# Kernel optimization log

Hardware: AMD Instinct MI355X
Metric: run time of the kernel (lower is better)

## Reference

```python
import jax, jax.numpy as jnp
import numpy as np

LAYERS = 30
LAYERS_PER_STACK = 10  # layers // stacks
UPSAMPLE_SCALES = (10, 8)


def _c1x1(w, x):
    # 1x1 conv: w [O,C], x [B,C,T] -> [B,O,T]
    return jnp.einsum('oc,bct->bot', w, x)


def setup_inputs() -> dict:
    key = jax.random.key(0)
    ks = jax.random.split(key, 16)
    B, T, F = 4, 32000, 400
    s = 0.1  # weight scale to keep gates unsaturated
    inp = {
        'x': jax.random.normal(ks[0], (B, 256, T), jnp.float32),
        'c': jax.random.normal(ks[1], (B, 80, F), jnp.float32),
        'first_w': jax.random.normal(ks[2], (64, 256), jnp.float32) * s,
        'first_b': jnp.zeros((64,), jnp.float32),
        'conv_w': jax.random.normal(ks[3], (LAYERS, 128, 64, 2), jnp.float32) * s,
        'conv_b': jnp.zeros((LAYERS, 128), jnp.float32),
        'cond_w': jax.random.normal(ks[4], (LAYERS, 128, 80), jnp.float32) * s,
        'out_w': jax.random.normal(ks[5], (LAYERS, 64, 64), jnp.float32) * s,
        'out_b': jnp.zeros((LAYERS, 64), jnp.float32),
        'skip_w': jax.random.normal(ks[6], (LAYERS, 64, 64), jnp.float32) * s,
        'skip_b': jnp.zeros((LAYERS, 64), jnp.float32),
        'last1_w': jax.random.normal(ks[7], (64, 64), jnp.float32) * s,
        'last1_b': jnp.zeros((64,), jnp.float32),
        'last2_w': jax.random.normal(ks[8], (256, 64), jnp.float32) * s,
        'last2_b': jnp.zeros((256,), jnp.float32),
        'conv_in_w': jax.random.normal(ks[9], (80, 80), jnp.float32) * s,
        # upsample smoothing kernels, torch init: constant 1/kernel_size
        'up_w0': jnp.full((2 * 10 + 1,), 1.0 / (2 * 10 + 1), jnp.float32),
        'up_w1': jnp.full((2 * 8 + 1,), 1.0 / (2 * 8 + 1), jnp.float32),
    }
    return inp


def _wavenet(x, c, first_w, first_b, conv_w, conv_b, cond_w, out_w, out_b,
             skip_w, skip_b, last1_w, last1_b, last2_w, last2_b, conv_in_w,
             up_w0, up_w1):
    # --- ConvInUpsampleNetwork (aux_context_window=0 -> conv_in is 1x1, no bias) ---
    c = _c1x1(conv_in_w, c)  # [B,80,F]
    C = c.shape[1]
    for scale, w in zip(UPSAMPLE_SCALES, (up_w0, up_w1)):
        c = jnp.repeat(c, scale, axis=2)  # nearest interpolate along time
        rhs = jnp.broadcast_to(w[None, None, :], (C, 1, w.shape[0]))  # depthwise avg
        c = jax.lax.conv_general_dilated(
            c, rhs, window_strides=(1,), padding=[(scale, scale)],
            feature_group_count=C, dimension_numbers=('NCH', 'OIH', 'NCH'))
    # c now [B,80,T] with T = F*80 matching x
    T = x.shape[2]

    # --- first 1x1 conv ---
    h = _c1x1(first_w, x) + first_b[None, :, None]  # [B,64,T]

    skips = jnp.zeros_like(h[:, :64, :]) * 0.0  # [B,64,T]
    skips = 0.0
    for l in range(LAYERS):
        d = 2 ** (l % LAYERS_PER_STACK)  # dilation; padding = (k-1)*d = d
        xp = jnp.pad(h, ((0, 0), (0, 0), (d, 0)))  # causal left pad
        # dilated conv, kernel_size=2: taps at t-d and t
        g = (jnp.einsum('oc,bct->bot', conv_w[l, :, :, 0], xp[:, :, :T])
             + jnp.einsum('oc,bct->bot', conv_w[l, :, :, 1], xp[:, :, d:d + T])
             + conv_b[l][None, :, None])  # [B,128,T]
        g = g + _c1x1(cond_w[l], c)  # conditioning (split(a,b)+split(ca,cb) == split(g+cc))
        a, b = jnp.split(g, 2, axis=1)
        z = jnp.tanh(a) * jax.nn.sigmoid(b)  # [B,64,T]
        skips = skips + _c1x1(skip_w[l], z) + skip_b[l][None, :, None]
        h = h + _c1x1(out_w[l], z) + out_b[l][None, :, None]

    # --- last conv layers: ReLU, 1x1, ReLU, 1x1 ---
    o = jax.nn.relu(skips)
    o = _c1x1(last1_w, o) + last1_b[None, :, None]
    o = jax.nn.relu(o)
    o = _c1x1(last2_w, o) + last2_b[None, :, None]
    return o  # [B,256,T]


def reference(x, c, first_w, first_b, conv_w, conv_b, cond_w, out_w, out_b,
              skip_w, skip_b, last1_w, last1_b, last2_w, last2_b, conv_in_w,
              up_w0, up_w1):
    return _wavenet(x, c, first_w, first_b, conv_w, conv_b, cond_w, out_w,
                    out_b, skip_w, skip_b, last1_w, last1_b, last2_w, last2_b,
                    conv_in_w, up_w0, up_w1)
```

## Files before the change

### kernel.cpp

```cpp
#include <hip/hip_runtime.h>
#include <math.h>

#define T_TOTAL 32000
#define BATCH 4
#define TT 64

typedef __bf16 bf16x8 __attribute__((ext_vector_type(8)));
typedef float f32x4 __attribute__((ext_vector_type(4)));
typedef unsigned int uint4v __attribute__((ext_vector_type(4)));
typedef unsigned int uint2v __attribute__((ext_vector_type(2)));

__device__ __forceinline__ unsigned short f2b(float f) {
    unsigned int u = __float_as_uint(f);
    u += 0x7FFFu + ((u >> 16) & 1u);
    return (unsigned short)(u >> 16);
}
__device__ __forceinline__ unsigned int f2b2(float lo, float hi) {
    return (unsigned int)f2b(lo) | ((unsigned int)f2b(hi) << 16);
}
__device__ __forceinline__ bf16x8 ld_bf8(const unsigned short* p) {
    return __builtin_bit_cast(bf16x8, *(const uint4v*)p);
}
__device__ __forceinline__ float fast_sigmoid(float x) {
    return __builtin_amdgcn_rcpf(1.0f + __expf(-x));
}
__device__ __forceinline__ float fast_tanh(float x) {
    return 1.0f - 2.0f * __builtin_amdgcn_rcpf(1.0f + __expf(2.0f * x));
}

__global__ void k_pack(const float* __restrict__ conv_w, const float* __restrict__ cond_w,
                       const float* __restrict__ skip_w, const float* __restrict__ out_w,
                       const float* __restrict__ first_w, const float* __restrict__ last1_w,
                       const float* __restrict__ last2_w,
                       unsigned short* __restrict__ wgp, unsigned short* __restrict__ wzp,
                       unsigned short* __restrict__ fwp, unsigned short* __restrict__ l1p,
                       unsigned short* __restrict__ l2p) {
    int i = blockIdx.x * blockDim.x + threadIdx.x;
    if (i < 860160) {
        int l = i / 28672, r = i % 28672;
        int o = r / 224, k = r % 224;
        float v;
        if (k < 64)       v = conv_w[(((size_t)l * 128 + o) * 64 + k) * 2 + 0];
        else if (k < 128) v = conv_w[(((size_t)l * 128 + o) * 64 + (k - 64)) * 2 + 1];
        else if (k < 208) v = cond_w[((size_t)l * 128 + o) * 80 + (k - 128)];
        else              v = 0.0f;
        wgp[i] = f2b(v);
        return;
    }
    i -= 860160;
    if (i < 245760) {
        int l = i / 8192, rr = (i % 8192) / 64, k = i % 64;
        float v = (rr < 64) ? skip_w[((size_t)l * 64 + rr) * 64 + k]
                            : out_w[((size_t)l * 64 + (rr - 64)) * 64 + k];
        wzp[i] = f2b(v);
        return;
    }
    i -= 245760;
    if (i < 16384) { fwp[i] = f2b(first_w[i]); return; }
    i -= 16384;
    if (i < 4096) { l1p[i] = f2b(last1_w[i]); return; }
    i -= 4096;
    if (i < 16384) { l2p[i] = f2b(last2_w[i]); return; }
}

__global__ void k_convin(const float* __restrict__ c, const float* __restrict__ w,
                         float* __restrict__ c1) {
    int idx = blockIdx.x * blockDim.x + threadIdx.x;
    if (idx >= BATCH * 80 * 400) return;
    int f = idx % 400;
    int o = (idx / 400) % 80;
    int b = idx / (400 * 80);
    const float* cb = c + (size_t)b * 80 * 400 + f;
    const float* wr = w + o * 80;
    float acc = 0.f;
    #pragma unroll 8
    for (int j = 0; j < 80; ++j) acc += wr[j] * cb[(size_t)j * 400];
    c1[idx] = acc;
}

__global__ void k_up0(const float* __restrict__ c1, const float* __restrict__ w,
                      float* __restrict__ c2) {
    int idx = blockIdx.x * blockDim.x + threadIdx.x;
    if (idx >= BATCH * 80 * 4000) return;
    int t = idx % 4000;
    int ch = idx / 4000;
    int u = t / 10, r = t - u * 10;
    float w0 = 0.f, w1 = 0.f, w2 = 0.f;
    #pragma unroll
    for (int j = 0; j < 21; ++j) {
        float wj = w[j];
        int a = r - 10 + j;
        if (a < 0) w0 += wj;
        else if (a < 10) w1 += wj;
        else w2 += wj;
    }
    const float* src = c1 + (size_t)ch * 400;
    float s0 = (u >= 1) ? src[u - 1] : 0.f;
    float s1 = src[u];
    float s2 = (u + 1 < 400) ? src[u + 1] : 0.f;
    c2[idx] = w0 * s0 + w1 * s1 + w2 * s2;
}

__global__ __launch_bounds__(256) void k_up1b(const float* __restrict__ c2,
                                              const float* __restrict__ w,
                                              unsigned short* __restrict__ cupb) {
    __shared__ float S[80][13];
    __shared__ float W[8][4];
    const int b = blockIdx.y, t0 = blockIdx.x * 64;
    const int tid = threadIdx.x;
    const int u0 = t0 >> 3;

    for (int i = tid; i < 800; i += 256) {
        int ch = i / 10, uu = i % 10;
        int u = u0 - 1 + uu;
        float v = 0.f;
        if (u >= 0 && u < 4000) v = c2[((size_t)b * 80 + ch) * 4000 + u];
        S[ch][uu] = v;
    }
    if (tid < 24) {
        int r = tid / 3, k = tid % 3;
        int jlo = (k == 0) ? 0 : (k == 1 ? 8 - r : 16 - r);
        int jhi = (k == 0) ? 7 - r : (k == 1 ? 15 - r : 16);
        float a = 0.f;
        for (int j = jlo; j <= jhi; ++j) a += w[j];
        W[r][k] = a;
    }
    __syncthreads();

    unsigned short* ob = cupb + ((size_t)b * T_TOTAL + t0) * 96;
    for (int i = tid; i < 64 * 96; i += 256) {
        int ch = i % 96;
        int tl = i / 96;
        float acc = 0.f;
        if (ch < 80) {
            int r = tl & 7, ub = tl >> 3;
            acc = W[r][0] * S[ch][ub] + W[r][1] * S[ch][ub + 1] + W[r][2] * S[ch][ub + 2];
        }
        ob[i] = f2b(acc);
    }
}

__global__ __launch_bounds__(256, 4) void k_first(
    const float* __restrict__ x, const unsigned short* __restrict__ fwp,
    const float* __restrict__ fb, float* __restrict__ h0) {
    __shared__ unsigned short Xf[64 * 264];
    const int b = blockIdx.y, t0 = blockIdx.x * TT, tid = threadIdx.x;
    const int lane = tid & 63;
    const int wv = __builtin_amdgcn_readfirstlane(tid >> 6);
    const int l15 = lane & 15, q = lane >> 4;

    for (int i = tid; i < 2048; i += 256) {
        int tb = i >> 8, ch = i & 255;
        const float* xr = x + ((size_t)b * 256 + ch) * T_TOTAL + t0 + tb * 8;
        float4 u0 = *(const float4*)xr;
        float4 u1 = *(const float4*)(xr + 4);
        int base = (tb * 8) * 264 + ch;
        Xf[base + 0 * 264] = f2b(u0.x);
        Xf[base + 1 * 264] = f2b(u0.y);
        Xf[base + 2 * 264] = f2b(u0.z);
        Xf[base + 3 * 264] = f2b(u0.w);
        Xf[base + 4 * 264] = f2b(u1.x);
        Xf[base + 5 * 264] = f2b(u1.y);
        Xf[base + 6 * 264] = f2b(u1.z);
        Xf[base + 7 * 264] = f2b(u1.w);
    }
    __syncthreads();

    f32x4 acc[4] = {};
    const unsigned short* wr = fwp + (size_t)(16 * wv + l15) * 256;
    #pragma unroll
    for (int ks = 0; ks < 8; ++ks) {
        bf16x8 aA = ld_bf8(wr + ks * 32 + q * 8);
        #pragma unroll
        for (int tt = 0; tt < 4; ++tt) {
            bf16x8 bb = ld_bf8(&Xf[(tt * 16 + l15) * 264 + ks * 32 + q * 8]);
            acc[tt] = __builtin_amdgcn_mfma_f32_16x16x32_bf16(aA, bb, acc[tt], 0, 0, 0);
        }
    }
    const float4 fbv = *(const float4*)&fb[16 * wv + 4 * q];
    float* hob = h0 + (size_t)b * T_TOTAL * 64;
    #pragma unroll
    for (int tt = 0; tt < 4; ++tt) {
        size_t base = (size_t)(t0 + tt * 16 + l15) * 64 + 16 * wv + 4 * q;
        float4 ho;
        ho.x = acc[tt][0] + fbv.x;
        ho.y = acc[tt][1] + fbv.y;
        ho.z = acc[tt][2] + fbv.z;
        ho.w = acc[tt][3] + fbv.w;
        *(float4*)(hob + base) = ho;
    }
}

__global__ __launch_bounds__(256, 4) void k_layer(
    const float* __restrict__ h_in, float* __restrict__ h_out,
    float* __restrict__ skips, const unsigned short* __restrict__ cupb,
    const unsigned short* __restrict__ wgp, const unsigned short* __restrict__ wzp,
    const float* __restrict__ cb_l, const float* __restrict__ ob_l,
    const float* __restrict__ sb_l, int d, int first) {
    __shared__ unsigned short Xl[64 * 224];
    __shared__ unsigned short zs[64 * 72];
    const int b = blockIdx.y, t0 = blockIdx.x * TT, tid = threadIdx.x;
    const int lane = tid & 63;
    const int wv = __builtin_amdgcn_readfirstlane(tid >> 6);
    const int l15 = lane & 15, q = lane >> 4;

    const float* hb = h_in + (size_t)b * T_TOTAL * 64;
    for (int i = tid; i < 512; i += 256) {
        int t = i >> 3, cb8 = (i & 7) << 3;
        const float4* p1 = (const float4*)(hb + (size_t)(t0 + t) * 64 + cb8);
        float4 u0 = p1[0], u1 = p1[1];
        uint4v v1;
        v1.x = f2b2(u0.x, u0.y); v1.y = f2b2(u0.z, u0.w);
        v1.z = f2b2(u1.x, u1.y); v1.w = f2b2(u1.z, u1.w);
        *(uint4v*)&Xl[t * 224 + 64 + cb8] = v1;
        int td = t0 + t - d;
        uint4v v0 = {0u, 0u, 0u, 0u};
        if (td >= 0) {
            const float4* p0 = (const float4*)(hb + (size_t)td * 64 + cb8);
            float4 w0 = p0[0], w1 = p0[1];
            v0.x = f2b2(w0.x, w0.y); v0.y = f2b2(w0.z, w0.w);
            v0.z = f2b2(w1.x, w1.y); v0.w = f2b2(w1.z, w1.w);
        }
        *(uint4v*)&Xl[t * 224 + cb8] = v0;
    }
    const unsigned short* cbb = cupb + (size_t)b * T_TOTAL * 96;
    for (int i = tid; i < 768; i += 256) {
        int t = i / 12, j = (i % 12) << 3;
        *(uint4v*)&Xl[t * 224 + 128 + j] = *(const uint4v*)&cbb[(size_t)(t0 + t) * 96 + j];
    }
    __syncthreads();

    f32x4 accA[4] = {}, accG[4] = {};
    const unsigned short* wrow_a = wgp + (size_t)(16 * wv + l15) * 224;
    const unsigned short* wrow_g = wgp + (size_t)(64 + 16 * wv + l15) * 224;
    #pragma unroll
    for (int ks = 0; ks < 7; ++ks) {
        bf16x8 aA = ld_bf8(wrow_a + ks * 32 + q * 8);
        bf16x8 aG = ld_bf8(wrow_g + ks * 32 + q * 8);
        #pragma unroll
        for (int tt = 0; tt < 4; ++tt) {
            bf16x8 bb = ld_bf8(&Xl[(tt * 16 + l15) * 224 + ks * 32 + q * 8]);
            accA[tt] = __builtin_amdgcn_mfma_f32_16x16x32_bf16(aA, bb, accA[tt], 0, 0, 0);
            accG[tt] = __builtin_amdgcn_mfma_f32_16x16x32_bf16(aG, bb, accG[tt], 0, 0, 0);
        }
    }
    const float4 cbA = *(const float4*)&cb_l[16 * wv + 4 * q];
    const float4 cbG = *(const float4*)&cb_l[64 + 16 * wv + 4 * q];
    #pragma unroll
    for (int tt = 0; tt < 4; ++tt) {
        int t = tt * 16 + l15;
        float z0 = fast_tanh(accA[tt][0] + cbA.x) * fast_sigmoid(accG[tt][0] + cbG.x);
        float z1 = fast_tanh(accA[tt][1] + cbA.y) * fast_sigmoid(accG[tt][1] + cbG.y);
        float z2 = fast_tanh(accA[tt][2] + cbA.z) * fast_sigmoid(accG[tt][2] + cbG.z);
        float z3 = fast_tanh(accA[tt][3] + cbA.w) * fast_sigmoid(accG[tt][3] + cbG.w);
        uint2v zv;
        zv.x = f2b2(z0, z1);
        zv.y = f2b2(z2, z3);
        *(uint2v*)&zs[t * 72 + 16 * wv + 4 * q] = zv;
    }
    __syncthreads();

    f32x4 accS[4] = {}, accO[4] = {};
    const unsigned short* zrow_s = wzp + (size_t)(16 * wv + l15) * 64;
    const unsigned short* zrow_o = wzp + (size_t)(64 + 16 * wv + l15) * 64;
    #pragma unroll
    for (int ks = 0; ks < 2; ++ks) {
        bf16x8 aS = ld_bf8(zrow_s + ks * 32 + q * 8);
        bf16x8 aO = ld_bf8(zrow_o + ks * 32 + q * 8);
        #pragma unroll
        for (int tt = 0; tt < 4; ++tt) {
            bf16x8 bb = ld_bf8(&zs[(tt * 16 + l15) * 72 + ks * 32 + q * 8]);
            accS[tt] = __builtin_amdgcn_mfma_f32_16x16x32_bf16(aS, bb, accS[tt], 0, 0, 0);
            accO[tt] = __builtin_amdgcn_mfma_f32_16x16x32_bf16(aO, bb, accO[tt], 0, 0, 0);
        }
    }
    const float4 sbv = *(const float4*)&sb_l[16 * wv + 4 * q];
    const float4 obv = *(const float4*)&ob_l[16 * wv + 4 * q];
    float* hob = h_out + (size_t)b * T_TOTAL * 64;
    float* skb = skips + (size_t)b * T_TOTAL * 64;
    #pragma unroll
    for (int tt = 0; tt < 4; ++tt) {
        size_t base = (size_t)(t0 + tt * 16 + l15) * 64 + 16 * wv + 4 * q;
        float4 hi = *(const float4*)(hb + base);
        float4 ho;
        ho.x = hi.x + accO[tt][0] + obv.x;
        ho.y = hi.y + accO[tt][1] + obv.y;
        ho.z = hi.z + accO[tt][2] + obv.z;
        ho.w = hi.w + accO[tt][3] + obv.w;
        *(float4*)(hob + base) = ho;
        float4 sv;
        if (first) {
            sv.x = accS[tt][0] + sbv.x;
            sv.y = accS[tt][1] + sbv.y;
            sv.z = accS[tt][2] + sbv.z;
            sv.w = accS[tt][3] + sbv.w;
        } else {
            float4 sp = *(const float4*)(skb + base);
            sv.x = sp.x + accS[tt][0] + sbv.x;
            sv.y = sp.y + accS[tt][1] + sbv.y;
            sv.z = sp.z + accS[tt][2] + sbv.z;
            sv.w = sp.w + accS[tt][3] + sbv.w;
        }
        *(float4*)(skb + base) = sv;
    }
}

__global__ __launch_bounds__(256) void k_last(
    const float* __restrict__ skips, const unsigned short* __restrict__ l1p,
    const float* __restrict__ b1, const unsigned short* __restrict__ l2p,
    const float* __restrict__ b2, float* __restrict__ out) {
    __shared__ unsigned short sp[64 * 72];
    __shared__ unsigned short o2s[64 * 72];
    const int b = blockIdx.y, t0 = blockIdx.x * TT, tid = threadIdx.x;
    const int lane = tid & 63;
    const int wv = __builtin_amdgcn_readfirstlane(tid >> 6);
    const int l15 = lane & 15, q = lane >> 4;

    const float* skb = skips + (size_t)b * T_TOTAL * 64;
    for (int i = tid; i < 512; i += 256) {
        int t = i >> 3, cb8 = (i & 7) << 3;
        const float4* p = (const float4*)(skb + (size_t)(t0 + t) * 64 + cb8);
        float4 u0 = p[0], u1 = p[1];
        uint4v v;
        v.x = f2b2(fmaxf(u0.x, 0.f), fmaxf(u0.y, 0.f));
        v.y = f2b2(fmaxf(u0.z, 0.f), fmaxf(u0.w, 0.f));
        v.z = f2b2(fmaxf(u1.x, 0.f), fmaxf(u1.y, 0.f));
        v.w = f2b2(fmaxf(u1.z, 0.f), fmaxf(u1.w, 0.f));
        *(uint4v*)&sp[t * 72 + cb8] = v;
    }
    __syncthreads();

    f32x4 a1[4] = {};
    const unsigned short* w1r = l1p + (size_t)(16 * wv + l15) * 64;
    #pragma unroll
    for (int ks = 0; ks < 2; ++ks) {
        bf16x8 aA = ld_bf8(w1r + ks * 32 + q * 8);
        #pragma unroll
        for (int tt = 0; tt < 4; ++tt) {
            bf16x8 bb = ld_bf8(&sp[(tt * 16 + l15) * 72 + ks * 32 + q * 8]);
            a1[tt] = __builtin_amdgcn_mfma_f32_16x16x32_bf16(aA, bb, a1[tt], 0, 0, 0);
        }
    }
    const float4 b1v = *(const float4*)&b1[16 * wv + 4 * q];
    #pragma unroll
    for (int tt = 0; tt < 4; ++tt) {
        int t = tt * 16 + l15;
        float z0 = fmaxf(a1[tt][0] + b1v.x, 0.f);
        float z1 = fmaxf(a1[tt][1] + b1v.y, 0.f);
        float z2 = fmaxf(a1[tt][2] + b1v.z, 0.f);
        float z3 = fmaxf(a1[tt][3] + b1v.w, 0.f);
        uint2v zv;
        zv.x = f2b2(z0, z1);
        zv.y = f2b2(z2, z3);
        *(uint2v*)&o2s[t * 72 + 16 * wv + 4 * q] = zv;
    }
    __syncthreads();

    f32x4 a2[4][4] = {};
    #pragma unroll
    for (int ks = 0; ks < 2; ++ks) {
        bf16x8 aw[4];
        #pragma unroll
        for (int j = 0; j < 4; ++j)
            aw[j] = ld_bf8(l2p + (size_t)(64 * wv + 16 * j + l15) * 64 + ks * 32 + q * 8);
        #pragma unroll
        for (int tt = 0; tt < 4; ++tt) {
            bf16x8 bb = ld_bf8(&o2s[(tt * 16 + l15) * 72 + ks * 32 + q * 8]);
            #pragma unroll
            for (int j = 0; j < 4; ++j)
                a2[j][tt] = __builtin_amdgcn_mfma_f32_16x16x32_bf16(aw[j], bb, a2[j][tt], 0, 0, 0);
        }
    }
    float* ob = out + (size_t)b * 256 * T_TOTAL;
    #pragma unroll
    for (int j = 0; j < 4; ++j) {
        int o0 = 64 * wv + 16 * j + 4 * q;
        float4 b2v = *(const float4*)&b2[o0];
        #pragma unroll
        for (int tt = 0; tt < 4; ++tt) {
            int t = t0 + tt * 16 + l15;
            ob[(size_t)(o0 + 0) * T_TOTAL + t] = a2[j][tt][0] + b2v.x;
            ob[(size_t)(o0 + 1) * T_TOTAL + t] = a2[j][tt][1] + b2v.y;
            ob[(size_t)(o0 + 2) * T_TOTAL + t] = a2[j][tt][2] + b2v.z;
            ob[(size_t)(o0 + 3) * T_TOTAL + t] = a2[j][tt][3] + b2v.w;
        }
    }
}

extern "C" void kernel_launch(void* const* d_in, const int* in_sizes, int n_in,
                              void* d_out, int out_size, void* d_ws, size_t ws_size,
                              hipStream_t stream) {
    const float* x         = (const float*)d_in[0];
    const float* c         = (const float*)d_in[1];
    const float* first_w   = (const float*)d_in[2];
    const float* first_b   = (const float*)d_in[3];
    const float* conv_w    = (const float*)d_in[4];
    const float* conv_b    = (const float*)d_in[5];
    const float* cond_w    = (const float*)d_in[6];
    const float* out_w     = (const float*)d_in[7];
    const float* out_b     = (const float*)d_in[8];
    const float* skip_w    = (const float*)d_in[9];
    const float* skip_b    = (const float*)d_in[10];
    const float* last1_w   = (const float*)d_in[11];
    const float* last1_b   = (const float*)d_in[12];
    const float* last2_w   = (const float*)d_in[13];
    const float* last2_b   = (const float*)d_in[14];
    const float* conv_in_w = (const float*)d_in[15];
    const float* up_w0     = (const float*)d_in[16];
    const float* up_w1     = (const float*)d_in[17];

    unsigned char* base = (unsigned char*)d_ws;
    float* c1            = (float*)(base + 0);
    float* c2            = (float*)(base + 512000);
    unsigned short* cupb = (unsigned short*)(base + 5632000);
    float* hA            = (float*)(base + 30208000);
    float* hB            = (float*)(base + 62976000);
    float* skips         = (float*)(base + 95744000);
    unsigned short* wgp  = (unsigned short*)(base + 128512000);
    unsigned short* wzp  = (unsigned short*)(base + 130232320);
    unsigned short* fwp  = (unsigned short*)(base + 130723840);
    unsigned short* l1p  = (unsigned short*)(base + 130756608);
    unsigned short* l2p  = (unsigned short*)(base + 130764800);

    k_pack<<<(1142784 + 255) / 256, 256, 0, stream>>>(
        conv_w, cond_w, skip_w, out_w, first_w, last1_w, last2_w,
        wgp, wzp, fwp, l1p, l2p);
    k_convin<<<(BATCH * 80 * 400 + 255) / 256, 256, 0, stream>>>(c, conv_in_w, c1);
    k_up0<<<(BATCH * 80 * 4000 + 255) / 256, 256, 0, stream>>>(c1, up_w0, c2);
    dim3 upg(T_TOTAL / 64, BATCH);
    k_up1b<<<upg, 256, 0, stream>>>(c2, up_w1, cupb);

    dim3 grid(T_TOTAL / TT, BATCH);
    k_first<<<grid, 256, 0, stream>>>(x, fwp, first_b, hA);

    float* hin = hA;
    float* hout = hB;
    for (int l = 0; l < 30; ++l) {
        int d = 1 << (l % 10);
        k_layer<<<grid, 256, 0, stream>>>(
            hin, hout, skips, cupb,
            wgp + (size_t)l * 128 * 224, wzp + (size_t)l * 128 * 64,
            conv_b + (size_t)l * 128, out_b + (size_t)l * 64, skip_b + (size_t)l * 64,
            d, l == 0 ? 1 : 0);
        float* tmp = hin; hin = hout; hout = tmp;
    }

    k_last<<<grid, 256, 0, stream>>>(skips, l1p, last1_b, l2p, last2_b, (float*)d_out);
}
```

Baseline: 1.504 ms.

## Defer skip projections to a final kernel using per-layer bf16 gate outputs

When the workspace is large enough, each layer kernel writes its gated activation z to a per-layer bf16 buffer instead of reading and writing the fp32 skips accumulator. A new k_skips kernel then accumulates all 30 skip projections in registers, adds the pre-summed skip bias, and runs the two output convolutions. This removes the per-layer fp32 read-modify-write of skips, at the cost of about 490 MB of extra workspace and one large final read. Separately, k_first loads one float4 per thread and pads its shared-memory row stride to 266 to reduce bank conflicts. If the workspace is too small, the old path is kept as a fallback.

Measured after the change: 1.493 ms. About the same (-0.7%).

```diff
diff --git a/kernel.cpp b/kernel.cpp
--- a/kernel.cpp
+++ b/kernel.cpp
@@ -31,10 +31,10 @@
 __global__ void k_pack(const float* __restrict__ conv_w, const float* __restrict__ cond_w,
                        const float* __restrict__ skip_w, const float* __restrict__ out_w,
                        const float* __restrict__ first_w, const float* __restrict__ last1_w,
-                       const float* __restrict__ last2_w,
+                       const float* __restrict__ last2_w, const float* __restrict__ skip_b,
                        unsigned short* __restrict__ wgp, unsigned short* __restrict__ wzp,
                        unsigned short* __restrict__ fwp, unsigned short* __restrict__ l1p,
-                       unsigned short* __restrict__ l2p) {
+                       unsigned short* __restrict__ l2p, float* __restrict__ sbs, int do_sbs) {
     int i = blockIdx.x * blockDim.x + threadIdx.x;
     if (i < 860160) {
         int l = i / 28672, r = i % 28672;
@@ -61,6 +61,12 @@
     if (i < 4096) { l1p[i] = f2b(last1_w[i]); return; }
     i -= 4096;
     if (i < 16384) { l2p[i] = f2b(last2_w[i]); return; }
+    i -= 16384;
+    if (i < 64 && do_sbs) {
+        float a = 0.f;
+        for (int l = 0; l < 30; ++l) a += skip_b[l * 64 + i];
+        sbs[i] = a;
+    }
 }
 
 __global__ void k_convin(const float* __restrict__ c, const float* __restrict__ w,
@@ -140,29 +146,26 @@
     }
 }
 
+#define XFS 266
 __global__ __launch_bounds__(256, 4) void k_first(
     const float* __restrict__ x, const unsigned short* __restrict__ fwp,
     const float* __restrict__ fb, float* __restrict__ h0) {
-    __shared__ unsigned short Xf[64 * 264];
+    __shared__ unsigned short Xf[64 * XFS];
     const int b = blockIdx.y, t0 = blockIdx.x * TT, tid = threadIdx.x;
     const int lane = tid & 63;
     const int wv = __builtin_amdgcn_readfirstlane(tid >> 6);
     const int l15 = lane & 15, q = lane >> 4;
 
-    for (int i = tid; i < 2048; i += 256) {
-        int tb = i >> 8, ch = i & 255;
-        const float* xr = x + ((size_t)b * 256 + ch) * T_TOTAL + t0 + tb * 8;
-        float4 u0 = *(const float4*)xr;
-        float4 u1 = *(const float4*)(xr + 4);
-        int base = (tb * 8) * 264 + ch;
-        Xf[base + 0 * 264] = f2b(u0.x);
-        Xf[base + 1 * 264] = f2b(u0.y);
-        Xf[base + 2 * 264] = f2b(u0.z);
-        Xf[base + 3 * 264] = f2b(u0.w);
-        Xf[base + 4 * 264] = f2b(u1.x);
-        Xf[base + 5 * 264] = f2b(u1.y);
-        Xf[base + 6 * 264] = f2b(u1.z);
-        Xf[base + 7 * 264] = f2b(u1.w);
+    for (int i = tid; i < 4096; i += 256) {
+        int ch = i >> 4;
+        int t4 = (i & 15) << 2;
+        const float* xr = x + ((size_t)b * 256 + ch) * T_TOTAL + t0 + t4;
+        float4 u = *(const float4*)xr;
+        int base = t4 * XFS + ch;
+        Xf[base + 0 * XFS] = f2b(u.x);
+        Xf[base + 1 * XFS] = f2b(u.y);
+        Xf[base + 2 * XFS] = f2b(u.z);
+        Xf[base + 3 * XFS] = f2b(u.w);
     }
     __syncthreads();
 
@@ -173,7 +176,7 @@
         bf16x8 aA = ld_bf8(wr + ks * 32 + q * 8);
         #pragma unroll
         for (int tt = 0; tt < 4; ++tt) {
-            bf16x8 bb = ld_bf8(&Xf[(tt * 16 + l15) * 264 + ks * 32 + q * 8]);
+            bf16x8 bb = ld_bf8(&Xf[(tt * 16 + l15) * XFS + ks * 32 + q * 8]);
             acc[tt] = __builtin_amdgcn_mfma_f32_16x16x32_bf16(aA, bb, acc[tt], 0, 0, 0);
         }
     }
@@ -192,6 +195,108 @@
 }
 
 __global__ __launch_bounds__(256, 4) void k_layer(
+    const float* __restrict__ h_in, float* __restrict__ h_out,
+    unsigned short* __restrict__ zb_l, const unsigned short* __restrict__ cupb,
+    const unsigned short* __restrict__ wgp_l, const unsigned short* __restrict__ wzp_l,
+    const float* __restrict__ cb_l, const float* __restrict__ ob_l, int d) {
+    __shared__ unsigned short Xl[64 * 224];
+    __shared__ unsigned short zs[64 * 72];
+    const int b = blockIdx.y, t0 = blockIdx.x * TT, tid = threadIdx.x;
+    const int lane = tid & 63;
+    const int wv = __builtin_amdgcn_readfirstlane(tid >> 6);
+    const int l15 = lane & 15, q = lane >> 4;
+
+    const float* hb = h_in + (size_t)b * T_TOTAL * 64;
+    for (int i = tid; i < 512; i += 256) {
+        int t = i >> 3, cb8 = (i & 7) << 3;
+        const float4* p1 = (const float4*)(hb + (size_t)(t0 + t) * 64 + cb8);
+        float4 u0 = p1[0], u1 = p1[1];
+        uint4v v1;
+        v1.x = f2b2(u0.x, u0.y); v1.y = f2b2(u0.z, u0.w);
+        v1.z = f2b2(u1.x, u1.y); v1.w = f2b2(u1.z, u1.w);
+        *(uint4v*)&Xl[t * 224 + 64 + cb8] = v1;
+        int td = t0 + t - d;
+        uint4v v0 = {0u, 0u, 0u, 0u};
+        if (td >= 0) {
+            const float4* p0 = (const float4*)(hb + (size_t)td * 64 + cb8);
+            float4 w0 = p0[0], w1 = p0[1];
+            v0.x = f2b2(w0.x, w0.y); v0.y = f2b2(w0.z, w0.w);
+            v0.z = f2b2(w1.x, w1.y); v0.w = f2b2(w1.z, w1.w);
+        }
+        *(uint4v*)&Xl[t * 224 + cb8] = v0;
+    }
+    const unsigned short* cbb = cupb + (size_t)b * T_TOTAL * 96;
+    for (int i = tid; i < 768; i += 256) {
+        int t = i / 12, j = (i % 12) << 3;
+        *(uint4v*)&Xl[t * 224 + 128 + j] = *(const uint4v*)&cbb[(size_t)(t0 + t) * 96 + j];
+    }
+    __syncthreads();
+
+    f32x4 accA[4] = {}, accG[4] = {};
+    const unsigned short* wrow_a = wgp_l + (size_t)(16 * wv + l15) * 224;
+    const unsigned short* wrow_g = wgp_l + (size_t)(64 + 16 * wv + l15) * 224;
+    #pragma unroll
+    for (int ks = 0; ks < 7; ++ks) {
+        bf16x8 aA = ld_bf8(wrow_a + ks * 32 + q * 8);
+        bf16x8 aG = ld_bf8(wrow_g + ks * 32 + q * 8);
+        #pragma unroll
+        for (int tt = 0; tt < 4; ++tt) {
+            bf16x8 bb = ld_bf8(&Xl[(tt * 16 + l15) * 224 + ks * 32 + q * 8]);
+            accA[tt] = __builtin_amdgcn_mfma_f32_16x16x32_bf16(aA, bb, accA[tt], 0, 0, 0);
+            accG[tt] = __builtin_amdgcn_mfma_f32_16x16x32_bf16(aG, bb, accG[tt], 0, 0, 0);
+        }
+    }
+    const float4 cbA = *(const float4*)&cb_l[16 * wv + 4 * q];
+    const float4 cbG = *(const float4*)&cb_l[64 + 16 * wv + 4 * q];
+    #pragma unroll
+    for (int tt = 0; tt < 4; ++tt) {
+        int t = tt * 16 + l15;
+        float z0 = fast_tanh(accA[tt][0] + cbA.x) * fast_sigmoid(accG[tt][0] + cbG.x);
+        float z1 = fast_tanh(accA[tt][1] + cbA.y) * fast_sigmoid(accG[tt][1] + cbG.y);
+        float z2 = fast_tanh(accA[tt][2] + cbA.z) * fast_sigmoid(accG[tt][2] + cbG.z);
+        float z3 = fast_tanh(accA[tt][3] + cbA.w) * fast_sigmoid(accG[tt][3] + cbG.w);
+        uint2v zv;
+        zv.x = f2b2(z0, z1);
+        zv.y = f2b2(z2, z3);
+        *(uint2v*)&zs[t * 72 + 16 * wv + 4 * q] = zv;
+    }
+    __syncthreads();
+
+    unsigned short* zg = zb_l + ((size_t)b * T_TOTAL + t0) * 64;
+    #pragma unroll
+    for (int it = 0; it < 2; ++it) {
+        int i = tid + it * 256;
+        int t = i >> 3, c8 = (i & 7) << 3;
+        *(uint4v*)&zg[t * 64 + c8] = *(const uint4v*)&zs[t * 72 + c8];
+    }
+
+    f32x4 accO[4] = {};
+    const unsigned short* zrow_o = wzp_l + (size_t)(64 + 16 * wv + l15) * 64;
+    #pragma unroll
+    for (int ks = 0; ks < 2; ++ks) {
+        bf16x8 aO = ld_bf8(zrow_o + ks * 32 + q * 8);
+        #pragma unroll
+        for (int tt = 0; tt < 4; ++tt) {
+            bf16x8 bb = ld_bf8(&zs[(tt * 16 + l15) * 72 + ks * 32 + q * 8]);
+            accO[tt] = __builtin_amdgcn_mfma_f32_16x16x32_bf16(aO, bb, accO[tt], 0, 0, 0);
+        }
+    }
+    const float4 obv = *(const float4*)&ob_l[16 * wv + 4 * q];
+    float* hob = h_out + (size_t)b * T_TOTAL * 64;
+    #pragma unroll
+    for (int tt = 0; tt < 4; ++tt) {
+        size_t base = (size_t)(t0 + tt * 16 + l15) * 64 + 16 * wv + 4 * q;
+        float4 hi = *(const float4*)(hb + base);
+        float4 ho;
+        ho.x = hi.x + accO[tt][0] + obv.x;
+        ho.y = hi.y + accO[tt][1] + obv.y;
+        ho.z = hi.z + accO[tt][2] + obv.z;
+        ho.w = hi.w + accO[tt][3] + obv.w;
+        *(float4*)(hob + base) = ho;
+    }
+}
+
+__global__ __launch_bounds__(256, 4) void k_layer_f(
     const float* __restrict__ h_in, float* __restrict__ h_out,
     float* __restrict__ skips, const unsigned short* __restrict__ cupb,
     const unsigned short* __restrict__ wgp, const unsigned short* __restrict__ wzp,
@@ -305,6 +410,113 @@
     }
 }
 
+__global__ __launch_bounds__(256) void k_skips(
+    const unsigned short* __restrict__ zbuf, const unsigned short* __restrict__ wzp,
+    const float* __restrict__ sbs, const unsigned short* __restrict__ l1p,
+    const float* __restrict__ b1, const unsigned short* __restrict__ l2p,
+    const float* __restrict__ b2, float* __restrict__ out) {
+    __shared__ unsigned short zt[64 * 72];
+    __shared__ unsigned short o2s[64 * 72];
+    const int b = blockIdx.y, t0 = blockIdx.x * TT, tid = threadIdx.x;
+    const int lane = tid & 63;
+    const int wv = __builtin_amdgcn_readfirstlane(tid >> 6);
+    const int l15 = lane & 15, q = lane >> 4;
+
+    const int st_t = tid >> 3, st_c = (tid & 7) << 3;
+    const int st_t2 = (tid + 256) >> 3, st_c2 = ((tid + 256) & 7) << 3;
+    const unsigned short* zb = zbuf + ((size_t)b * T_TOTAL + t0) * 64;
+
+    f32x4 acc[4] = {};
+    for (int l = 0; l < 30; ++l) {
+        const unsigned short* src = zb + (size_t)l * BATCH * T_TOTAL * 64;
+        *(uint4v*)&zt[st_t * 72 + st_c] = *(const uint4v*)&src[st_t * 64 + st_c];
+        *(uint4v*)&zt[st_t2 * 72 + st_c2] = *(const uint4v*)&src[st_t2 * 64 + st_c2];
+        __syncthreads();
+        const unsigned short* wr = wzp + (size_t)l * 8192 + (size_t)(16 * wv + l15) * 64;
+        #pragma unroll
+        for (int ks = 0; ks < 2; ++ks) {
+            bf16x8 aS = ld_bf8(wr + ks * 32 + q * 8);
+            #pragma unroll
+            for (int tt = 0; tt < 4; ++tt) {
+                bf16x8 bb = ld_bf8(&zt[(tt * 16 + l15) * 72 + ks * 32 + q * 8]);
+                acc[tt] = __builtin_amdgcn_mfma_f32_16x16x32_bf16(aS, bb, acc[tt], 0, 0, 0);
+            }
+        }
+        __syncthreads();
+    }
+
+    const float4 sbv = *(const float4*)&sbs[16 * wv + 4 * q];
+    #pragma unroll
+    for (int tt = 0; tt < 4; ++tt) {
+        int t = tt * 16 + l15;
+        float s0 = fmaxf(acc[tt][0] + sbv.x, 0.f);
+        float s1 = fmaxf(acc[tt][1] + sbv.y, 0.f);
+        float s2 = fmaxf(acc[tt][2] + sbv.z, 0.f);
+        float s3 = fmaxf(acc[tt][3] + sbv.w, 0.f);
+        uint2v zv;
+        zv.x = f2b2(s0, s1);
+        zv.y = f2b2(s2, s3);
+        *(uint2v*)&zt[t * 72 + 16 * wv + 4 * q] = zv;
+    }
+    __syncthreads();
+
+    f32x4 a1[4] = {};
+    const unsigned short* w1r = l1p + (size_t)(16 * wv + l15) * 64;
+    #pragma unroll
+    for (int ks = 0; ks < 2; ++ks) {
+        bf16x8 aA = ld_bf8(w1r + ks * 32 + q * 8);
+        #pragma unroll
+        for (int tt = 0; tt < 4; ++tt) {
+            bf16x8 bb = ld_bf8(&zt[(tt * 16 + l15) * 72 + ks * 32 + q * 8]);
+            a1[tt] = __builtin_amdgcn_mfma_f32_16x16x32_bf16(aA, bb, a1[tt], 0, 0, 0);
+        }
+    }
+    const float4 b1v = *(const float4*)&b1[16 * wv + 4 * q];
+    #pragma unroll
+    for (int tt = 0; tt < 4; ++tt) {
+        int t = tt * 16 + l15;
+        float z0 = fmaxf(a1[tt][0] + b1v.x, 0.f);
+        float z1 = fmaxf(a1[tt][1] + b1v.y, 0.f);
+        float z2 = fmaxf(a1[tt][2] + b1v.z, 0.f);
+        float z3 = fmaxf(a1[tt][3] + b1v.w, 0.f);
+        uint2v zv;
+        zv.x = f2b2(z0, z1);
+        zv.y = f2b2(z2, z3);
+        *(uint2v*)&o2s[t * 72 + 16 * wv + 4 * q] = zv;
+    }
+    __syncthreads();
+
+    f32x4 a2[4][4] = {};
+    #pragma unroll
+    for (int ks = 0; ks < 2; ++ks) {
+        bf16x8 aw[4];
+        #pragma unroll
+        for (int j = 0; j < 4; ++j)
+            aw[j] = ld_bf8(l2p + (size_t)(64 * wv + 16 * j + l15) * 64 + ks * 32 + q * 8);
+        #pragma unroll
+        for (int tt = 0; tt < 4; ++tt) {
+            bf16x8 bb = ld_bf8(&o2s[(tt * 16 + l15) * 72 + ks * 32 + q * 8]);
+            #pragma unroll
+            for (int j = 0; j < 4; ++j)
+                a2[j][tt] = __builtin_amdgcn_mfma_f32_16x16x32_bf16(aw[j], bb, a2[j][tt], 0, 0, 0);
+        }
+    }
+    float* ob = out + (size_t)b * 256 * T_TOTAL;
+    #pragma unroll
+    for (int j = 0; j < 4; ++j) {
+        int o0 = 64 * wv + 16 * j + 4 * q;
+        float4 b2v = *(const float4*)&b2[o0];
+        #pragma unroll
+        for (int tt = 0; tt < 4; ++tt) {
+            int t = t0 + tt * 16 + l15;
+            ob[(size_t)(o0 + 0) * T_TOTAL + t] = a2[j][tt][0] + b2v.x;
+            ob[(size_t)(o0 + 1) * T_TOTAL + t] = a2[j][tt][1] + b2v.y;
+            ob[(size_t)(o0 + 2) * T_TOTAL + t] = a2[j][tt][2] + b2v.z;
+            ob[(size_t)(o0 + 3) * T_TOTAL + t] = a2[j][tt][3] + b2v.w;
+        }
+    }
+}
+
 __global__ __launch_bounds__(256) void k_last(
     const float* __restrict__ skips, const unsigned short* __restrict__ l1p,
     const float* __restrict__ b1, const unsigned short* __restrict__ l2p,
@@ -410,40 +622,82 @@
     const float* up_w1     = (const float*)d_in[17];
 
     unsigned char* base = (unsigned char*)d_ws;
-    float* c1            = (float*)(base + 0);
-    float* c2            = (float*)(base + 512000);
-    unsigned short* cupb = (unsigned short*)(base + 5632000);
-    float* hA            = (float*)(base + 30208000);
-    float* hB            = (float*)(base + 62976000);
-    float* skips         = (float*)(base + 95744000);
-    unsigned short* wgp  = (unsigned short*)(base + 128512000);
-    unsigned short* wzp  = (unsigned short*)(base + 130232320);
-    unsigned short* fwp  = (unsigned short*)(base + 130723840);
-    unsigned short* l1p  = (unsigned short*)(base + 130756608);
-    unsigned short* l2p  = (unsigned short*)(base + 130764800);
-
-    k_pack<<<(1142784 + 255) / 256, 256, 0, stream>>>(
-        conv_w, cond_w, skip_w, out_w, first_w, last1_w, last2_w,
-        wgp, wzp, fwp, l1p, l2p);
-    k_convin<<<(BATCH * 80 * 400 + 255) / 256, 256, 0, stream>>>(c, conv_in_w, c1);
-    k_up0<<<(BATCH * 80 * 4000 + 255) / 256, 256, 0, stream>>>(c1, up_w0, c2);
+    const size_t NEED_BIG = 589549824ull;
+    const bool big = ws_size >= NEED_BIG;
+
+    dim3 grid(T_TOTAL / TT, BATCH);
     dim3 upg(T_TOTAL / 64, BATCH);
-    k_up1b<<<upg, 256, 0, stream>>>(c2, up_w1, cupb);
-
-    dim3 grid(T_TOTAL / TT, BATCH);
-    k_first<<<grid, 256, 0, stream>>>(x, fwp, first_b, hA);
-
-    float* hin = hA;
-    float* hout = hB;
-    for (int l = 0; l < 30; ++l) {
-        int d = 1 << (l % 10);
-        k_layer<<<grid, 256, 0, stream>>>(
-            hin, hout, skips, cupb,
-            wgp + (size_t)l * 128 * 224, wzp + (size_t)l * 128 * 64,
-            conv_b + (size_t)l * 128, out_b + (size_t)l * 64, skip_b + (size_t)l * 64,
-            d, l == 0 ? 1 : 0);
-        float* tmp = hin; hin = hout; hout = tmp;
-    }
-
-    k_last<<<grid, 256, 0, stream>>>(skips, l1p, last1_b, l2p, last2_b, (float*)d_out);
-}
+
+    if (big) {
+        float* c1            = (float*)(base + 0);
+        float* c2            = (float*)(base + 512000);
+        unsigned short* cupb = (unsigned short*)(base + 5632000);
+        float* hA            = (float*)(base + 30208000);
+        float* hB            = (float*)(base + 62976000);
+        unsigned short* wgp  = (unsigned short*)(base + 95744000);
+        unsigned short* wzp  = (unsigned short*)(base + 97464320);
+        unsigned short* fwp  = (unsigned short*)(base + 97955840);
+        unsigned short* l1p  = (unsigned short*)(base + 97988608);
+        unsigned short* l2p  = (unsigned short*)(base + 97996800);
+        float* sbs           = (float*)(base + 98029568);
+        unsigned short* zbuf = (unsigned short*)(base + 98029824);
+
+        k_pack<<<(1142848 + 255) / 256, 256, 0, stream>>>(
+            conv_w, cond_w, skip_w, out_w, first_w, last1_w, last2_w, skip_b,
+            wgp, wzp, fwp, l1p, l2p, sbs, 1);
+        k_convin<<<(BATCH * 80 * 400 + 255) / 256, 256, 0, stream>>>(c, conv_in_w, c1);
+        k_up0<<<(BATCH * 80 * 4000 + 255) / 256, 256, 0, stream>>>(c1, up_w0, c2);
+        k_up1b<<<upg, 256, 0, stream>>>(c2, up_w1, cupb);
+
+        k_first<<<grid, 256, 0, stream>>>(x, fwp, first_b, hA);
+
+        float* hin = hA;
+        float* hout = hB;
+        for (int l = 0; l < 30; ++l) {
+            int d = 1 << (l % 10);
+            k_layer<<<grid, 256, 0, stream>>>(
+                hin, hout, zbuf + (size_t)l * BATCH * T_TOTAL * 64, cupb,
+                wgp + (size_t)l * 128 * 224, wzp + (size_t)l * 128 * 64,
+                conv_b + (size_t)l * 128, out_b + (size_t)l * 64, d);
+            float* tmp = hin; hin = hout; hout = tmp;
+        }
+
+        k_skips<<<grid, 256, 0, stream>>>(zbuf, wzp, sbs, l1p, last1_b, l2p, last2_b,
+                                          (float*)d_out);
+    } else {
+        float* c1            = (float*)(base + 0);
+        float* c2            = (float*)(base + 512000);
+        unsigned short* cupb = (unsigned short*)(base + 5632000);
+        float* hA            = (float*)(base + 30208000);
+        float* hB            = (float*)(base + 62976000);
+        float* skips         = (float*)(base + 95744000);
+        unsigned short* wgp  = (unsigned short*)(base + 128512000);
+        unsigned short* wzp  = (unsigned short*)(base + 130232320);
+        unsigned short* fwp  = (unsigned short*)(base + 130723840);
+        unsigned short* l1p  = (unsigned short*)(base + 130756608);
+        unsigned short* l2p  = (unsigned short*)(base + 130764800);
+
+        k_pack<<<(1142848 + 255) / 256, 256, 0, stream>>>(
+            conv_w, cond_w, skip_w, out_w, first_w, last1_w, last2_w, skip_b,
+            wgp, wzp, fwp, l1p, l2p, (float*)base, 0);
+        k_convin<<<(BATCH * 80 * 400 + 255) / 256, 256, 0, stream>>>(c, conv_in_w, c1);
+        k_up0<<<(BATCH * 80 * 4000 + 255) / 256, 256, 0, stream>>>(c1, up_w0, c2);
+        k_up1b<<<upg, 256, 0, stream>>>(c2, up_w1, cupb);
+
+        k_first<<<grid, 256, 0, stream>>>(x, fwp, first_b, hA);
+
+        float* hin = hA;
+        float* hout = hB;
+        for (int l = 0; l < 30; ++l) {
+            int d = 1 << (l % 10);
+            k_layer_f<<<grid, 256, 0, stream>>>(
+                hin, hout, skips, cupb,
+                wgp + (size_t)l * 128 * 224, wzp + (size_t)l * 128 * 64,
+                conv_b + (size_t)l * 128, out_b + (size_t)l * 64, skip_b + (size_t)l * 64,
+                d, l == 0 ? 1 : 0);
+            float* tmp = hin; hin = hout; hout = tmp;
+        }
+
+        k_last<<<grid, 256, 0, stream>>>(skips, l1p, last1_b, l2p, last2_b, (float*)d_out);
+    }
+}
```
